# Kernel tuning notes

Hardware: AMD Instinct MI355X
Metric: run time of the kernel (lower is better)

The kernel has to match this reference:

```python
import jax, jax.numpy as jnp
import numpy as np

B, T, D, R, V = 8, 512, 1024, 4, 2048


def setup_inputs() -> dict:
    key = jax.random.key(0)
    k1, k2, k3, k4, k5 = jax.random.split(key, 5)
    return {
        "input_embs": jax.random.normal(k1, (B, T, D), dtype=jnp.float32),
        "label_ids": jax.random.randint(k2, (B, T), 0, V),
        "w_alpha": jax.random.normal(k3, (D, R), dtype=jnp.float32),
        "w_beta": jax.random.normal(k4, (D, R), dtype=jnp.float32),
        "w_vocab": jax.random.normal(k5, (D, V * R * R), dtype=jnp.float32),
    }


def _normalize(m, axis):
    # torch normalize_matrix: abs then divide by sum over `dim` (rows of the matrix)
    m = jnp.abs(m)
    return m / m.sum(axis=axis, keepdims=True)


def reference(input_embs, label_ids, w_alpha, w_beta, w_vocab):
    x = input_embs
    Bq, Tq, Dq = x.shape
    xf = x.reshape(-1, Dq)                                   # [B*T, D]
    alpha = (xf @ w_alpha).reshape(Bq, Tq, R).mean(1)        # [B, R]
    beta = (xf @ w_beta).reshape(Bq, Tq, R).mean(1)          # [B, R]
    core = (xf @ w_vocab).reshape(Bq, Tq, R, V, R).mean(1)   # [B, R, V, R]

    # gather core slices core[b, :, y[b,k], :] -> [B, T, R, R]
    g = jnp.take_along_axis(core.transpose(0, 2, 1, 3),      # [B, V, R, R]
                            label_ids[:, :, None, None], axis=1)
    Mn = _normalize(g, axis=2)                               # normalize over matrix rows (dim=0)

    v = _normalize(alpha, axis=1)                            # [B, R] normalized column vector
    Ms = Mn.transpose(1, 0, 2, 3)                            # [T, B, R, R]

    def step(v, M):
        return jnp.einsum('bij,bj->bi', M, v), None

    v, _ = jax.lax.scan(step, v, Ms)                         # sequential TT chain over T
    nb = _normalize(beta, axis=1)                            # [B, R]
    probs = jnp.einsum('bi,bi->b', nb, v)                    # [B]
    loss = -jnp.log(probs)
    return loss.mean()
```

## Files before the change

kernel.cpp:

```cpp
#include <hip/hip_runtime.h>
#include <math.h>

#define Bq 8
#define T 512
#define D 1024
#define R 4
#define V 2048
#define NCOL (V * R * R)
#define DSPLIT 16
#define DCHUNK (D / DSPLIT)
#define CBLK 1024
#define NTC 32

__global__ void k_xbar(const float* __restrict__ x, float* __restrict__ partial,
                       float* __restrict__ out) {
    int b   = blockIdx.x;
    int tc  = blockIdx.y;
    int tid = threadIdx.x;
    if (b == 0 && tc == 0 && tid == 0) out[0] = 0.f;
    const float4* xp = (const float4*)(x + ((size_t)b * T + (size_t)tc * 16) * D) + tid;
    float4 acc = make_float4(0.f, 0.f, 0.f, 0.f);
#pragma unroll
    for (int t = 0; t < 16; ++t) {
        float4 v = xp[t * (D / 4)];
        acc.x += v.x; acc.y += v.y; acc.z += v.z; acc.w += v.w;
    }
    *(float4*)(partial + ((size_t)b * NTC + tc) * D + tid * 4) = acc;
}

__global__ void k_core(const float* __restrict__ wv, const float* __restrict__ partial,
                       float* __restrict__ xbar, float* __restrict__ part) {
    __shared__ float xs[Bq * DCHUNK];
    int tid  = threadIdx.x;
    int colb = blockIdx.x;
    int ds   = blockIdx.y;
    int d0   = ds * DCHUNK;

#pragma unroll
    for (int h = 0; h < 2; ++h) {
        int q  = tid + h * 256;
        int b  = q >> 6;
        int dd = q & 63;
        const float* pp = partial + (size_t)b * NTC * D + d0 + dd;
        float s = 0.f;
#pragma unroll
        for (int tc = 0; tc < NTC; ++tc) s += pp[(size_t)tc * D];
        xs[q] = s;
    }
    __syncthreads();

    if (colb == 0 && tid < 128) {
        int q4 = tid * 4;
        int b  = q4 >> 6;
        int dd = q4 & 63;
        *(float4*)(xbar + b * D + d0 + dd) = *(const float4*)(xs + q4);
    }

    int col = colb * CBLK + tid * 4;
    const float4* wp = (const float4*)(wv + (size_t)d0 * NCOL + col);
    float4 acc[Bq];
#pragma unroll
    for (int b = 0; b < Bq; ++b) acc[b] = make_float4(0.f, 0.f, 0.f, 0.f);

#pragma unroll 8
    for (int d = 0; d < DCHUNK; ++d) {
        float4 w = wp[(size_t)d * (NCOL / 4)];
#pragma unroll
        for (int b = 0; b < Bq; ++b) {
            float xv = xs[b * DCHUNK + d];
            acc[b].x += w.x * xv;
            acc[b].y += w.y * xv;
            acc[b].z += w.z * xv;
            acc[b].w += w.w * xv;
        }
    }

#pragma unroll
    for (int b = 0; b < Bq; ++b)
        *(float4*)(part + ((size_t)ds * Bq + b) * NCOL + col) = acc[b];
}

__global__ void k_gather(const float* __restrict__ part, const int* __restrict__ labels,
                         float* __restrict__ Mn) {
    int b   = blockIdx.x;
    int tc  = blockIdx.y;
    int tid = threadIdx.x;
    int tl  = tid >> 2;
    int i   = tid & 3;
    int t   = tc * 64 + tl;
    int y   = labels[b * T + t];

    const float* pb = part + (size_t)b * NCOL + (size_t)i * (V * R) + (size_t)y * R;
    float4 g = make_float4(0.f, 0.f, 0.f, 0.f);
#pragma unroll
    for (int ds = 0; ds < DSPLIT; ++ds) {
        float4 v = *(const float4*)(pb + (size_t)ds * (Bq * NCOL));
        g.x += v.x; g.y += v.y; g.z += v.z; g.w += v.w;
    }
    g.x = fabsf(g.x); g.y = fabsf(g.y); g.z = fabsf(g.z); g.w = fabsf(g.w);

    float sx = g.x, sy = g.y, sz = g.z, sw = g.w;
    sx += __shfl_xor(sx, 1); sy += __shfl_xor(sy, 1);
    sz += __shfl_xor(sz, 1); sw += __shfl_xor(sw, 1);
    sx += __shfl_xor(sx, 2); sy += __shfl_xor(sy, 2);
    sz += __shfl_xor(sz, 2); sw += __shfl_xor(sw, 2);

    float4 o = make_float4(g.x / sx, g.y / sy, g.z / sz, g.w / sw);
    *(float4*)(Mn + ((size_t)(b * T + t)) * 16 + i * 4) = o;
}

__global__ void k_chain(const float* __restrict__ Mn, const float* __restrict__ xbar,
                        const float* __restrict__ wa, const float* __restrict__ wb,
                        float* __restrict__ out) {
    __shared__ float mats[64][17];
    __shared__ float abp[64];
    int b   = blockIdx.x;
    int tid = threadIdx.x;

    {
        int r   = tid & 3;
        int sel = (tid >> 2) & 1;
        int seg = tid >> 3;
        const float* w  = sel ? wb : wa;
        const float* xp = xbar + b * D;
        float s = 0.f;
#pragma unroll 8
        for (int d = seg * 128; d < seg * 128 + 128; ++d)
            s += xp[d] * w[d * R + r];
        abp[tid] = s;
    }

    int c = tid;
    const float* mp = Mn + ((size_t)b * T + (size_t)c * 8) * 16;
    float P[R][R];
    {
        float4 m0 = *(const float4*)(mp + 0);
        float4 m1 = *(const float4*)(mp + 4);
        float4 m2 = *(const float4*)(mp + 8);
        float4 m3 = *(const float4*)(mp + 12);
        P[0][0]=m0.x; P[0][1]=m0.y; P[0][2]=m0.z; P[0][3]=m0.w;
        P[1][0]=m1.x; P[1][1]=m1.y; P[1][2]=m1.z; P[1][3]=m1.w;
        P[2][0]=m2.x; P[2][1]=m2.y; P[2][2]=m2.z; P[2][3]=m2.w;
        P[3][0]=m3.x; P[3][1]=m3.y; P[3][2]=m3.z; P[3][3]=m3.w;
    }
#pragma unroll
    for (int t = 1; t < 8; ++t) {
        float4 m0 = *(const float4*)(mp + t * 16 + 0);
        float4 m1 = *(const float4*)(mp + t * 16 + 4);
        float4 m2 = *(const float4*)(mp + t * 16 + 8);
        float4 m3 = *(const float4*)(mp + t * 16 + 12);
        float M[R][R] = {{m0.x, m0.y, m0.z, m0.w},
                         {m1.x, m1.y, m1.z, m1.w},
                         {m2.x, m2.y, m2.z, m2.w},
                         {m3.x, m3.y, m3.z, m3.w}};
        float N[R][R];
#pragma unroll
        for (int i = 0; i < R; ++i)
#pragma unroll
            for (int j = 0; j < R; ++j)
                N[i][j] = M[i][0] * P[0][j] + M[i][1] * P[1][j] +
                          M[i][2] * P[2][j] + M[i][3] * P[3][j];
#pragma unroll
        for (int i = 0; i < R; ++i)
#pragma unroll
            for (int j = 0; j < R; ++j) P[i][j] = N[i][j];
    }
#pragma unroll
    for (int i = 0; i < R; ++i)
#pragma unroll
        for (int j = 0; j < R; ++j) mats[c][i * 4 + j] = P[i][j];
    __syncthreads();

    for (int rnd = 0; rnd < 6; ++rnd) {
        int step = 1 << rnd;
        bool act = ((c & (2 * step - 1)) == 0);
        float N2[R][R];
        if (act) {
            float A[R][R], Bm[R][R];
#pragma unroll
            for (int i = 0; i < R; ++i)
#pragma unroll
                for (int j = 0; j < R; ++j) {
                    A[i][j]  = mats[c + step][i * 4 + j];
                    Bm[i][j] = mats[c][i * 4 + j];
                }
#pragma unroll
            for (int i = 0; i < R; ++i)
#pragma unroll
                for (int j = 0; j < R; ++j)
                    N2[i][j] = A[i][0] * Bm[0][j] + A[i][1] * Bm[1][j] +
                               A[i][2] * Bm[2][j] + A[i][3] * Bm[3][j];
        }
        __syncthreads();
        if (act) {
#pragma unroll
            for (int i = 0; i < R; ++i)
#pragma unroll
                for (int j = 0; j < R; ++j) mats[c][i * 4 + j] = N2[i][j];
        }
        __syncthreads();
    }

    if (tid == 0) {
        float a[R], be[R];
#pragma unroll
        for (int r = 0; r < R; ++r) {
            float sa = 0.f, sb = 0.f;
#pragma unroll
            for (int seg = 0; seg < 8; ++seg) {
                sa += abp[(seg << 3) | r];
                sb += abp[(seg << 3) | 4 | r];
            }
            a[r] = sa; be[r] = sb;
        }
        float sa = fabsf(a[0]) + fabsf(a[1]) + fabsf(a[2]) + fabsf(a[3]);
        float v0[R];
#pragma unroll
        for (int r = 0; r < R; ++r) v0[r] = fabsf(a[r]) / sa;
        float v[R];
#pragma unroll
        for (int i = 0; i < R; ++i)
            v[i] = mats[0][i * 4 + 0] * v0[0] + mats[0][i * 4 + 1] * v0[1] +
                   mats[0][i * 4 + 2] * v0[2] + mats[0][i * 4 + 3] * v0[3];
        float sb = fabsf(be[0]) + fabsf(be[1]) + fabsf(be[2]) + fabsf(be[3]);
        float prob = (fabsf(be[0]) * v[0] + fabsf(be[1]) * v[1] +
                      fabsf(be[2]) * v[2] + fabsf(be[3]) * v[3]) / sb;
        atomicAdd(out, -logf(prob) * 0.125f);
    }
}

extern "C" void kernel_launch(void* const* d_in, const int* in_sizes, int n_in,
                              void* d_out, int out_size, void* d_ws, size_t ws_size,
                              hipStream_t stream) {
    const float* x      = (const float*)d_in[0];
    const int*   labels = (const int*)d_in[1];
    const float* wa     = (const float*)d_in[2];
    const float* wb     = (const float*)d_in[3];
    const float* wv     = (const float*)d_in[4];
    float* out = (float*)d_out;

    float* xbar    = (float*)d_ws;
    float* partial = xbar + Bq * D;
    float* part    = partial + (size_t)Bq * NTC * D;
    float* Mn      = part + (size_t)DSPLIT * Bq * NCOL;

    k_xbar<<<dim3(Bq, NTC), 256, 0, stream>>>(x, partial, out);
    k_core<<<dim3(NCOL / CBLK, DSPLIT), 256, 0, stream>>>(wv, partial, xbar, part);
    k_gather<<<dim3(Bq, T / 64), 256, 0, stream>>>(part, labels, Mn);
    k_chain<<<Bq, 64, 0, stream>>>(Mn, xbar, wa, wb, out);
}
```

Measured before the change: 232.9 us.

## Skip stores of unused vocab columns and fuse chunk matrix products into gather

k_core now builds a per-batch label bitmask in shared memory and writes partial core results only for vocab entries that appear in the labels, which cuts the large partial-sum write traffic. k_gather now multiplies its 64 normalized matrices in shared memory, so it emits one product per 64-step chunk instead of the full Mn array, and k_chain only combines 8 products. Each k_core block pays extra label loads and shared atomics, and skipped entries are left unwritten in the workspace.

```diff
diff --git a/kernel.cpp b/kernel.cpp
--- a/kernel.cpp
+++ b/kernel.cpp
@@ -29,12 +29,16 @@
 }
 
 __global__ void k_core(const float* __restrict__ wv, const float* __restrict__ partial,
+                       const int* __restrict__ labels,
                        float* __restrict__ xbar, float* __restrict__ part) {
     __shared__ float xs[Bq * DCHUNK];
+    __shared__ unsigned int msk[Bq * 64];
     int tid  = threadIdx.x;
     int colb = blockIdx.x;
     int ds   = blockIdx.y;
     int d0   = ds * DCHUNK;
+
+    msk[tid] = 0u; msk[tid + 256] = 0u;
 
 #pragma unroll
     for (int h = 0; h < 2; ++h) {
@@ -49,14 +53,24 @@
     }
     __syncthreads();
 
+#pragma unroll
+    for (int h = 0; h < 16; ++h) {
+        int idx = tid * 16 + h;
+        int b   = idx >> 9;
+        int y   = labels[idx];
+        atomicOr(&msk[b * 64 + (y >> 5)], 1u << (y & 31));
+    }
+
     if (colb == 0 && tid < 128) {
         int q4 = tid * 4;
         int b  = q4 >> 6;
         int dd = q4 & 63;
         *(float4*)(xbar + b * D + d0 + dd) = *(const float4*)(xs + q4);
     }
+    __syncthreads();
 
     int col = colb * CBLK + tid * 4;
+    int y   = (colb * 256 + tid) & (V - 1);
     const float4* wp = (const float4*)(wv + (size_t)d0 * NCOL + col);
     float4 acc[Bq];
 #pragma unroll
@@ -76,12 +90,16 @@
     }
 
 #pragma unroll
-    for (int b = 0; b < Bq; ++b)
-        *(float4*)(part + ((size_t)ds * Bq + b) * NCOL + col) = acc[b];
+    for (int b = 0; b < Bq; ++b) {
+        if ((msk[b * 64 + (y >> 5)] >> (y & 31)) & 1u)
+            *(float4*)(part + ((size_t)ds * Bq + b) * NCOL + col) = acc[b];
+    }
 }
 
 __global__ void k_gather(const float* __restrict__ part, const int* __restrict__ labels,
-                         float* __restrict__ Mn) {
+                         float* __restrict__ bprod) {
+    __shared__ float Mn_s[64 * 16];
+    __shared__ float gm[8][17];
     int b   = blockIdx.x;
     int tc  = blockIdx.y;
     int tid = threadIdx.x;
@@ -106,13 +124,91 @@
     sz += __shfl_xor(sz, 2); sw += __shfl_xor(sw, 2);
 
     float4 o = make_float4(g.x / sx, g.y / sy, g.z / sz, g.w / sw);
-    *(float4*)(Mn + ((size_t)(b * T + t)) * 16 + i * 4) = o;
-}
-
-__global__ void k_chain(const float* __restrict__ Mn, const float* __restrict__ xbar,
+    *(float4*)(Mn_s + tl * 16 + i * 4) = o;
+    __syncthreads();
+
+    int c = tid;
+    if (c < 8) {
+        const float* mp = Mn_s + c * 8 * 16;
+        float P[R][R];
+        {
+            float4 m0 = *(const float4*)(mp + 0);
+            float4 m1 = *(const float4*)(mp + 4);
+            float4 m2 = *(const float4*)(mp + 8);
+            float4 m3 = *(const float4*)(mp + 12);
+            P[0][0]=m0.x; P[0][1]=m0.y; P[0][2]=m0.z; P[0][3]=m0.w;
+            P[1][0]=m1.x; P[1][1]=m1.y; P[1][2]=m1.z; P[1][3]=m1.w;
+            P[2][0]=m2.x; P[2][1]=m2.y; P[2][2]=m2.z; P[2][3]=m2.w;
+            P[3][0]=m3.x; P[3][1]=m3.y; P[3][2]=m3.z; P[3][3]=m3.w;
+        }
+#pragma unroll
+        for (int k = 1; k < 8; ++k) {
+            float4 m0 = *(const float4*)(mp + k * 16 + 0);
+            float4 m1 = *(const float4*)(mp + k * 16 + 4);
+            float4 m2 = *(const float4*)(mp + k * 16 + 8);
+            float4 m3 = *(const float4*)(mp + k * 16 + 12);
+            float M[R][R] = {{m0.x, m0.y, m0.z, m0.w},
+                             {m1.x, m1.y, m1.z, m1.w},
+                             {m2.x, m2.y, m2.z, m2.w},
+                             {m3.x, m3.y, m3.z, m3.w}};
+            float N[R][R];
+#pragma unroll
+            for (int ii = 0; ii < R; ++ii)
+#pragma unroll
+                for (int j = 0; j < R; ++j)
+                    N[ii][j] = M[ii][0] * P[0][j] + M[ii][1] * P[1][j] +
+                               M[ii][2] * P[2][j] + M[ii][3] * P[3][j];
+#pragma unroll
+            for (int ii = 0; ii < R; ++ii)
+#pragma unroll
+                for (int j = 0; j < R; ++j) P[ii][j] = N[ii][j];
+        }
+#pragma unroll
+        for (int ii = 0; ii < R; ++ii)
+#pragma unroll
+            for (int j = 0; j < R; ++j) gm[c][ii * 4 + j] = P[ii][j];
+    }
+    __syncthreads();
+
+    for (int rnd = 0; rnd < 3; ++rnd) {
+        int step = 1 << rnd;
+        bool act = (c < 8) && ((c & (2 * step - 1)) == 0);
+        float N2[R][R];
+        if (act) {
+            float A[R][R], Bm[R][R];
+#pragma unroll
+            for (int ii = 0; ii < R; ++ii)
+#pragma unroll
+                for (int j = 0; j < R; ++j) {
+                    A[ii][j]  = gm[c + step][ii * 4 + j];
+                    Bm[ii][j] = gm[c][ii * 4 + j];
+                }
+#pragma unroll
+            for (int ii = 0; ii < R; ++ii)
+#pragma unroll
+                for (int j = 0; j < R; ++j)
+                    N2[ii][j] = A[ii][0] * Bm[0][j] + A[ii][1] * Bm[1][j] +
+                                A[ii][2] * Bm[2][j] + A[ii][3] * Bm[3][j];
+        }
+        __syncthreads();
+        if (act) {
+#pragma unroll
+            for (int ii = 0; ii < R; ++ii)
+#pragma unroll
+                for (int j = 0; j < R; ++j) gm[c][ii * 4 + j] = N2[ii][j];
+        }
+        __syncthreads();
+    }
+
+    if (tid < 4)
+        *(float4*)(bprod + ((size_t)(b * 8 + tc)) * 16 + tid * 4) =
+            *(const float4*)(&gm[0][tid * 4]);
+}
+
+__global__ void k_chain(const float* __restrict__ bprod, const float* __restrict__ xbar,
                         const float* __restrict__ wa, const float* __restrict__ wb,
                         float* __restrict__ out) {
-    __shared__ float mats[64][17];
+    __shared__ float mats[8][17];
     __shared__ float abp[64];
     int b   = blockIdx.x;
     int tid = threadIdx.x;
@@ -130,50 +226,17 @@
         abp[tid] = s;
     }
 
+    if (tid < 32) {
+        int c = tid >> 2, q = tid & 3;
+        *(float4*)(&mats[c][q * 4]) =
+            *(const float4*)(bprod + ((size_t)(b * 8 + c)) * 16 + q * 4);
+    }
+    __syncthreads();
+
     int c = tid;
-    const float* mp = Mn + ((size_t)b * T + (size_t)c * 8) * 16;
-    float P[R][R];
-    {
-        float4 m0 = *(const float4*)(mp + 0);
-        float4 m1 = *(const float4*)(mp + 4);
-        float4 m2 = *(const float4*)(mp + 8);
-        float4 m3 = *(const float4*)(mp + 12);
-        P[0][0]=m0.x; P[0][1]=m0.y; P[0][2]=m0.z; P[0][3]=m0.w;
-        P[1][0]=m1.x; P[1][1]=m1.y; P[1][2]=m1.z; P[1][3]=m1.w;
-        P[2][0]=m2.x; P[2][1]=m2.y; P[2][2]=m2.z; P[2][3]=m2.w;
-        P[3][0]=m3.x; P[3][1]=m3.y; P[3][2]=m3.z; P[3][3]=m3.w;
-    }
-#pragma unroll
-    for (int t = 1; t < 8; ++t) {
-        float4 m0 = *(const float4*)(mp + t * 16 + 0);
-        float4 m1 = *(const float4*)(mp + t * 16 + 4);
-        float4 m2 = *(const float4*)(mp + t * 16 + 8);
-        float4 m3 = *(const float4*)(mp + t * 16 + 12);
-        float M[R][R] = {{m0.x, m0.y, m0.z, m0.w},
-                         {m1.x, m1.y, m1.z, m1.w},
-                         {m2.x, m2.y, m2.z, m2.w},
-                         {m3.x, m3.y, m3.z, m3.w}};
-        float N[R][R];
-#pragma unroll
-        for (int i = 0; i < R; ++i)
-#pragma unroll
-            for (int j = 0; j < R; ++j)
-                N[i][j] = M[i][0] * P[0][j] + M[i][1] * P[1][j] +
-                          M[i][2] * P[2][j] + M[i][3] * P[3][j];
-#pragma unroll
-        for (int i = 0; i < R; ++i)
-#pragma unroll
-            for (int j = 0; j < R; ++j) P[i][j] = N[i][j];
-    }
-#pragma unroll
-    for (int i = 0; i < R; ++i)
-#pragma unroll
-        for (int j = 0; j < R; ++j) mats[c][i * 4 + j] = P[i][j];
-    __syncthreads();
-
-    for (int rnd = 0; rnd < 6; ++rnd) {
+    for (int rnd = 0; rnd < 3; ++rnd) {
         int step = 1 << rnd;
-        bool act = ((c & (2 * step - 1)) == 0);
+        bool act = (c < 8) && ((c & (2 * step - 1)) == 0);
         float N2[R][R];
         if (act) {
             float A[R][R], Bm[R][R];
@@ -242,10 +305,10 @@
     float* xbar    = (float*)d_ws;
     float* partial = xbar + Bq * D;
     float* part    = partial + (size_t)Bq * NTC * D;
-    float* Mn      = part + (size_t)DSPLIT * Bq * NCOL;
+    float* bprod   = part + (size_t)DSPLIT * Bq * NCOL;
 
     k_xbar<<<dim3(Bq, NTC), 256, 0, stream>>>(x, partial, out);
-    k_core<<<dim3(NCOL / CBLK, DSPLIT), 256, 0, stream>>>(wv, partial, xbar, part);
-    k_gather<<<dim3(Bq, T / 64), 256, 0, stream>>>(part, labels, Mn);
-    k_chain<<<Bq, 64, 0, stream>>>(Mn, xbar, wa, wb, out);
-}
+    k_core<<<dim3(NCOL / CBLK, DSPLIT), 256, 0, stream>>>(wv, partial, labels, xbar, part);
+    k_gather<<<dim3(Bq, 8), 256, 0, stream>>>(part, labels, bprod);
+    k_chain<<<Bq, 64, 0, stream>>>(bprod, xbar, wa, wb, out);
+}
```

Result: slower. 241.2 us (+3.6%).
